# Kernel optimization log

Hardware: AMD Instinct MI355X
Metric: run time of the kernel (lower is better)

Reference implementation:

```python
import jax, jax.numpy as jnp
import numpy as np

NUM_ITER = 2
NUM_SLOTS = 3
D = 64          # slot_dim
MLP_H = 64
C_IN = 512
N = 262144      # number of input features (pixels)
EPS = 1e-8
LN_EPS = 1e-3   # keras LayerNormalization default


def _ln(x, g, b):
    m = jnp.mean(x, axis=-1, keepdims=True)
    v = jnp.var(x, axis=-1, keepdims=True)
    return (x - m) * jax.lax.rsqrt(v + LN_EPS) * g + b


def _gru(x, h, k, rk, bias):
    # keras GRUCell, reset_after=True; bias: [2, 3D] (input bias, recurrent bias)
    xm = x @ k + bias[0]
    hm = h @ rk + bias[1]
    xz, xr, xh = jnp.split(xm, 3, axis=-1)
    hz, hr, hh = jnp.split(hm, 3, axis=-1)
    z = jax.nn.sigmoid(xz + hz)
    r = jax.nn.sigmoid(xr + hr)
    cand = jnp.tanh(xh + r * hh)
    return z * h + (1.0 - z) * cand


def _mlp(s, g, b, W1, b1, W2, b2):
    h = _ln(s, g, b)
    return jax.nn.relu(h @ W1 + b1) @ W2 + b2


def _glorot(key, shape):
    fan_in, fan_out = shape[0], shape[-1]
    lim = np.sqrt(6.0 / (fan_in + fan_out))
    return jax.random.uniform(key, shape, jnp.float32, -lim, lim)


def setup_inputs() -> dict:
    key = jax.random.key(0)
    ks = jax.random.split(key, 24)
    inp = {
        'x': jax.random.normal(ks[0], (N, C_IN), jnp.float32),
        'noise_fg': jax.random.normal(ks[1], (NUM_SLOTS - 1, D), jnp.float32),
        'noise_bg': jax.random.normal(ks[2], (1, D), jnp.float32),
        'ln_g': jnp.ones((C_IN,), jnp.float32),
        'ln_b': jnp.zeros((C_IN,), jnp.float32),
        'mu_fg': _glorot(ks[3], (1, D)),
        'ls_fg': _glorot(ks[4], (1, D)),
        'mu_bg': _glorot(ks[5], (1, D)),
        'ls_bg': _glorot(ks[6], (1, D)),
        'Wk': _glorot(ks[7], (C_IN, D)),
        'Wv': _glorot(ks[8], (C_IN, D)),
        'qfg_g': jnp.ones((D,), jnp.float32), 'qfg_b': jnp.zeros((D,), jnp.float32),
        'qfg_W': _glorot(ks[9], (D, D)),
        'qbg_g': jnp.ones((D,), jnp.float32), 'qbg_b': jnp.zeros((D,), jnp.float32),
        'qbg_W': _glorot(ks[10], (D, D)),
        'grufg_k': _glorot(ks[11], (D, 3 * D)),
        'grufg_rk': _glorot(ks[12], (D, 3 * D)),
        'grufg_bias': jnp.zeros((2, 3 * D), jnp.float32),
        'grubg_k': _glorot(ks[13], (D, 3 * D)),
        'grubg_rk': _glorot(ks[14], (D, 3 * D)),
        'grubg_bias': jnp.zeros((2, 3 * D), jnp.float32),
        'mlpfg_g': jnp.ones((D,), jnp.float32), 'mlpfg_b': jnp.zeros((D,), jnp.float32),
        'mlpfg_W1': _glorot(ks[15], (D, MLP_H)), 'mlpfg_b1': jnp.zeros((MLP_H,), jnp.float32),
        'mlpfg_W2': _glorot(ks[16], (MLP_H, D)), 'mlpfg_b2': jnp.zeros((D,), jnp.float32),
        'mlpbg_g': jnp.ones((D,), jnp.float32), 'mlpbg_b': jnp.zeros((D,), jnp.float32),
        'mlpbg_W1': _glorot(ks[17], (D, MLP_H)), 'mlpbg_b1': jnp.zeros((MLP_H,), jnp.float32),
        'mlpbg_W2': _glorot(ks[18], (MLP_H, D)), 'mlpbg_b2': jnp.zeros((D,), jnp.float32),
    }
    return inp


def reference(x, noise_fg, noise_bg, ln_g, ln_b, mu_fg, ls_fg, mu_bg, ls_bg,
              Wk, Wv, qfg_g, qfg_b, qfg_W, qbg_g, qbg_b, qbg_W,
              grufg_k, grufg_rk, grufg_bias, grubg_k, grubg_rk, grubg_bias,
              mlpfg_g, mlpfg_b, mlpfg_W1, mlpfg_b1, mlpfg_W2, mlpfg_b2,
              mlpbg_g, mlpbg_b, mlpbg_W1, mlpbg_b1, mlpbg_W2, mlpbg_b2):
    x = _ln(x, ln_g, ln_b)
    slots_fg = mu_fg + jnp.exp(ls_fg) * noise_fg      # [K-1, D]
    slots_bg = mu_bg + jnp.exp(ls_bg) * noise_bg      # [1, D]
    k = x @ Wk                                        # [N, D]
    v = x @ Wv                                        # [N, D]
    scale = D ** (-0.5)
    attn = None
    for _ in range(NUM_ITER):
        q_fg = _ln(slots_fg, qfg_g, qfg_b) @ qfg_W * scale
        q_bg = _ln(slots_bg, qbg_g, qbg_b) @ qbg_W * scale
        logits = jnp.concatenate([k @ q_bg.T, k @ q_fg.T], axis=-1)  # [N, K]
        attn = jax.nn.softmax(logits, axis=-1)
        attn_bg, attn_fg = attn[:, 0:1], attn[:, 1:]
        w_bg = attn_bg + EPS
        w_bg = w_bg / jnp.sum(w_bg, axis=-2, keepdims=True)
        upd_bg = w_bg.T @ v                                          # [1, D]
        w_fg = attn_fg + EPS
        w_fg = w_fg / jnp.sum(w_fg, axis=-2, keepdims=True)
        upd_fg = w_fg.T @ v                                          # [K-1, D]
        slots_bg = _gru(upd_bg, slots_bg, grubg_k, grubg_rk, grubg_bias)
        slots_fg = _gru(upd_fg, slots_fg, grufg_k, grufg_rk, grufg_bias)
        slots_bg = slots_bg + _mlp(slots_bg, mlpbg_g, mlpbg_b, mlpbg_W1, mlpbg_b1, mlpbg_W2, mlpbg_b2)
        slots_fg = slots_fg + _mlp(slots_fg, mlpfg_g, mlpfg_b, mlpfg_W1, mlpfg_b1, mlpfg_W2, mlpfg_b2)
    slots = jnp.concatenate([slots_bg, slots_fg], axis=0)            # [K, D]
    return slots, attn.T                                             # [K,D], [K,N]
```

## Files before the change

kernel.cpp:

```cpp
#include <hip/hip_runtime.h>
#include <hip/hip_bf16.h>


#define N_TOK 262144
#define CIN 512
#define TILE_M 64
#define NBLK_A 512
#define NBLK_I2 1024
#define PSTRIDE 1024

typedef __attribute__((ext_vector_type(8))) short short8;
typedef __attribute__((ext_vector_type(4))) float f32x4;

__device__ __forceinline__ unsigned short f2bf(float f) {
    union { float f; unsigned u; } v; v.f = f;
    unsigned r = v.u + 0x7FFFu + ((v.u >> 16) & 1u);
    return (unsigned short)(r >> 16);
}
__device__ __forceinline__ unsigned pkbf(float a, float b) {
    return (unsigned)f2bf(a) | ((unsigned)f2bf(b) << 16);
}
__device__ __forceinline__ float bf2f(unsigned short u) {
    union { unsigned u; float f; } v; v.u = ((unsigned)u) << 16;
    return v.f;
}
__device__ __forceinline__ float sigmoidf_(float x) { return 1.f / (1.f + expf(-x)); }

__device__ __forceinline__ float q_from_slot(float v, const float* __restrict__ g,
                                             const float* __restrict__ b,
                                             const float* __restrict__ W, int lane) {
    float s = v, s2 = v * v;
#pragma unroll
    for (int d = 1; d < 64; d <<= 1) { s += __shfl_xor(s, d); s2 += __shfl_xor(s2, d); }
    float mean = s * (1.f / 64.f);
    float var = s2 * (1.f / 64.f) - mean * mean;
    float rstd = rsqrtf(var + 1e-3f);
    float hl = (v - mean) * rstd * g[lane] + b[lane];
    float acc = 0.f;
    for (int i = 0; i < 64; ++i) acc += __shfl(hl, i) * W[i * 64 + lane];
    return acc * 0.125f;
}

__global__ __launch_bounds__(256) void wt_init_kernel(
    const float* __restrict__ Wk, const float* __restrict__ Wv,
    const float* __restrict__ ln_g, const float* __restrict__ ln_b,
    unsigned short* __restrict__ Wt, float* __restrict__ c12,
    const float* __restrict__ noise_fg, const float* __restrict__ noise_bg,
    const float* __restrict__ mu_fg, const float* __restrict__ ls_fg,
    const float* __restrict__ mu_bg, const float* __restrict__ ls_bg,
    const float* __restrict__ qbg_g, const float* __restrict__ qbg_b, const float* __restrict__ qbg_W,
    const float* __restrict__ qfg_g, const float* __restrict__ qfg_b, const float* __restrict__ qfg_W,
    float* __restrict__ slots_ws, float* __restrict__ q_ws) {
    int t = threadIdx.x;
    if (blockIdx.x < 128) {
        int j = blockIdx.x;
        const float* W = (j < 64) ? Wk : Wv;
        int jc = j & 63;
        float c1 = 0.f, c2 = 0.f;
        for (int i = t; i < 512; i += 256) {
            float wv = W[i * 64 + jc];
            float g = ln_g[i], b = ln_b[i];
            c1 += g * wv; c2 += b * wv;
            Wt[(size_t)j * 512 + i] = f2bf(g * wv);
        }
        __shared__ float s1[4], s2[4];
#pragma unroll
        for (int d = 1; d < 64; d <<= 1) { c1 += __shfl_xor(c1, d); c2 += __shfl_xor(c2, d); }
        if ((t & 63) == 0) { s1[t >> 6] = c1; s2[t >> 6] = c2; }
        __syncthreads();
        if (t == 0) {
            c12[j] = (s1[0] + s1[1]) + (s1[2] + s1[3]);
            c12[128 + j] = (s2[0] + s2[1]) + (s2[2] + s2[3]);
        }
    } else {
        if (t < 192) {
            int s = t >> 6, c = t & 63;
            float v = (s == 0) ? (mu_bg[c] + expf(ls_bg[c]) * noise_bg[c])
                               : (mu_fg[c] + expf(ls_fg[c]) * noise_fg[(s - 1) * 64 + c]);
            slots_ws[t] = v;
            const float* g = s ? qfg_g : qbg_g;
            const float* b = s ? qfg_b : qbg_b;
            const float* W = s ? qfg_W : qbg_W;
            q_ws[t] = q_from_slot(v, g, b, W, c);
        }
    }
}

__global__ __launch_bounds__(256, 2) void phaseA_kernel(
    const float* __restrict__ x, const unsigned short* __restrict__ Wt,
    const float* __restrict__ c12, const float* __restrict__ qv,
    unsigned short* __restrict__ kb, unsigned short* __restrict__ vb,
    float* __restrict__ partials) {
    __shared__ unsigned short SA[TILE_M * CIN];
    __shared__ float q_s[192];
    __shared__ float w_s[64 * 4];
    __shared__ float2 rowstat[64];
    float* kvf = (float*)SA;

    const int t = threadIdx.x;
    const int lane = t & 63;
    const int w = t >> 6;

    if (t < 192) q_s[t] = qv[t];

    short8 bfrag[16][2];
    float c1r[2], c2r[2];
#pragma unroll
    for (int nt = 0; nt < 2; ++nt) {
        int col = w * 32 + nt * 16 + (lane & 15);
        c1r[nt] = c12[col];
        c2r[nt] = c12[128 + col];
#pragma unroll
        for (int kk = 0; kk < 16; ++kk) {
            int off = kk * 32 + ((lane >> 4) << 3);
            bfrag[kk][nt] = *(const short8*)(Wt + (size_t)col * 512 + off);
        }
    }

    float upd_acc = 0.f;
    float sw_acc = 0.f;

    for (int tile = blockIdx.x; tile < N_TOK / TILE_M; tile += NBLK_A) {
        const size_t row0 = (size_t)tile * TILE_M;
        __syncthreads();

#pragma unroll
        for (int p = 0; p < 2; ++p) {
            int r = w * 16 + p * 8 + (lane >> 3);
            int c8 = lane & 7;
            const float4* xr = (const float4*)(x + (row0 + r) * CIN) + c8 * 16;
            char* rowbase = (char*)SA + r * 1024;
            int bb = c8 * 128;
            int sw = (r & 7) << 4;
            float s = 0.f, s2 = 0.f;
#pragma unroll
            for (int i = 0; i < 8; ++i) {
                float4 a = xr[2 * i];
                float4 b = xr[2 * i + 1];
                s += (a.x + a.y) + (a.z + a.w) + (b.x + b.y) + (b.z + b.w);
                s2 = fmaf(a.x, a.x, s2); s2 = fmaf(a.y, a.y, s2);
                s2 = fmaf(a.z, a.z, s2); s2 = fmaf(a.w, a.w, s2);
                s2 = fmaf(b.x, b.x, s2); s2 = fmaf(b.y, b.y, s2);
                s2 = fmaf(b.z, b.z, s2); s2 = fmaf(b.w, b.w, s2);
                uint4 o;
                o.x = pkbf(a.x, a.y); o.y = pkbf(a.z, a.w);
                o.z = pkbf(b.x, b.y); o.w = pkbf(b.z, b.w);
                *(uint4*)(rowbase + ((bb + i * 16) ^ sw)) = o;
            }
#pragma unroll
            for (int d = 1; d < 8; d <<= 1) { s += __shfl_xor(s, d); s2 += __shfl_xor(s2, d); }
            if (c8 == 0) {
                float mean = s * (1.f / 512.f);
                float var = s2 * (1.f / 512.f) - mean * mean;
                float rstd = rsqrtf(var + 1e-3f);
                rowstat[r] = make_float2(rstd, mean * rstd);
            }
        }
        __syncthreads();

        f32x4 acc[4][2];
#pragma unroll
        for (int m = 0; m < 4; ++m) {
            acc[m][0] = (f32x4){0.f, 0.f, 0.f, 0.f};
            acc[m][1] = (f32x4){0.f, 0.f, 0.f, 0.f};
        }
#pragma unroll
        for (int kk = 0; kk < 16; ++kk) {
#pragma unroll
            for (int m = 0; m < 4; ++m) {
                int row = m * 16 + (lane & 15);
                int boff = (kk * 64 + ((lane >> 4) << 4)) ^ ((row & 7) << 4);
                short8 af = *(const short8*)((const char*)SA + row * 1024 + boff);
                acc[m][0] = __builtin_amdgcn_mfma_f32_16x16x32_bf16(af, bfrag[kk][0], acc[m][0], 0, 0, 0);
                acc[m][1] = __builtin_amdgcn_mfma_f32_16x16x32_bf16(af, bfrag[kk][1], acc[m][1], 0, 0, 0);
            }
        }
        __syncthreads();

        float2 rs[16];
#pragma unroll
        for (int m = 0; m < 4; ++m)
#pragma unroll
            for (int j = 0; j < 4; ++j)
                rs[m * 4 + j] = rowstat[m * 16 + ((lane >> 4) << 2) + j];
#pragma unroll
        for (int m = 0; m < 4; ++m)
#pragma unroll
            for (int n = 0; n < 2; ++n)
#pragma unroll
                for (int j = 0; j < 4; ++j) {
                    int row = m * 16 + ((lane >> 4) << 2) + j;
                    int col = w * 32 + n * 16 + (lane & 15);
                    float val = fmaf(rs[m * 4 + j].x, acc[m][n][j],
                                     fmaf(-rs[m * 4 + j].y, c1r[n], c2r[n]));
                    kvf[row * 130 + col] = val;
                }
        __syncthreads();

        {
            int r = t >> 2, q4 = t & 3;
            unsigned short* dst = ((q4 < 2) ? kb : vb) + (row0 + r) * 64 + (q4 & 1) * 32;
            const float* src = &kvf[r * 130 + q4 * 32];
#pragma unroll
            for (int j = 0; j < 32; j += 8) {
                float2 p0 = *(const float2*)(src + j);
                float2 p1 = *(const float2*)(src + j + 2);
                float2 p2 = *(const float2*)(src + j + 4);
                float2 p3 = *(const float2*)(src + j + 6);
                uint4 o;
                o.x = pkbf(p0.x, p0.y);
                o.y = pkbf(p1.x, p1.y);
                o.z = pkbf(p2.x, p2.y);
                o.w = pkbf(p3.x, p3.y);
                *(uint4*)(dst + j) = o;
            }
        }
        if (t < 64) {
            int r = t;
            float l0 = 0.f, l1 = 0.f, l2 = 0.f;
#pragma unroll 8
            for (int c = 0; c < 64; c += 2) {
                float2 kv2 = *(const float2*)&kvf[r * 130 + c];
                l0 += kv2.x * q_s[c] + kv2.y * q_s[c + 1];
                l1 += kv2.x * q_s[64 + c] + kv2.y * q_s[64 + c + 1];
                l2 += kv2.x * q_s[128 + c] + kv2.y * q_s[128 + c + 1];
            }
            float mx = fmaxf(l0, fmaxf(l1, l2));
            float e0 = expf(l0 - mx), e1 = expf(l1 - mx), e2 = expf(l2 - mx);
            float inv = 1.f / (e0 + e1 + e2);
            w_s[r * 4 + 0] = e0 * inv + 1e-8f;
            w_s[r * 4 + 1] = e1 * inv + 1e-8f;
            w_s[r * 4 + 2] = e2 * inv + 1e-8f;
        }
        __syncthreads();

        if (t < 192) {
            int s = t >> 6, c = t & 63;
            float a = 0.f;
            for (int r = 0; r < 64; ++r) a += w_s[r * 4 + s] * kvf[r * 130 + 64 + c];
            upd_acc += a;
        } else if (t < 195) {
            int s = t - 192;
            float a = 0.f;
            for (int r = 0; r < 64; ++r) a += w_s[r * 4 + s];
            sw_acc += a;
        }
    }
    if (t < 192) partials[(size_t)t * PSTRIDE + blockIdx.x] = upd_acc;
    else if (t < 195) partials[(size_t)t * PSTRIDE + blockIdx.x] = sw_acc;
}

__global__ __launch_bounds__(256) void iter2_kernel(
    const unsigned short* __restrict__ kb, const unsigned short* __restrict__ vb,
    const float* __restrict__ qv, float* __restrict__ attn_out, float* __restrict__ partials) {
    __shared__ float q_s[192];
    __shared__ float w_s[256 * 4];
    __shared__ unsigned short v_lds[256 * 64];
    int t = threadIdx.x;
    if (t < 192) q_s[t] = qv[t];
    __syncthreads();
    size_t r = (size_t)blockIdx.x * 256 + t;
    const unsigned short* krow = kb + r * 64;
    float l0 = 0.f, l1 = 0.f, l2 = 0.f;
#pragma unroll
    for (int i = 0; i < 8; ++i) {
        uint4 u = *(const uint4*)(krow + i * 8);
        unsigned uu[4] = {u.x, u.y, u.z, u.w};
#pragma unroll
        for (int p = 0; p < 4; ++p) {
            float fa = bf2f((unsigned short)(uu[p] & 0xffffu));
            float fb = bf2f((unsigned short)(uu[p] >> 16));
            int c = i * 8 + p * 2;
            l0 += fa * q_s[c] + fb * q_s[c + 1];
            l1 += fa * q_s[64 + c] + fb * q_s[64 + c + 1];
            l2 += fa * q_s[128 + c] + fb * q_s[128 + c + 1];
        }
    }
    float mx = fmaxf(l0, fmaxf(l1, l2));
    float e0 = expf(l0 - mx), e1 = expf(l1 - mx), e2 = expf(l2 - mx);
    float inv = 1.f / (e0 + e1 + e2);
    float a0 = e0 * inv, a1 = e1 * inv, a2 = e2 * inv;
    attn_out[r] = a0;
    attn_out[(size_t)N_TOK + r] = a1;
    attn_out[2 * (size_t)N_TOK + r] = a2;
    w_s[t * 4 + 0] = a0 + 1e-8f;
    w_s[t * 4 + 1] = a1 + 1e-8f;
    w_s[t * 4 + 2] = a2 + 1e-8f;
    {
        const uint4* vr = (const uint4*)(vb + r * 64);
        uint4* vl = (uint4*)(v_lds + t * 64);
#pragma unroll
        for (int i = 0; i < 8; ++i) vl[i] = vr[i];
    }
    __syncthreads();
    if (t < 192) {
        int s = t >> 6, c = t & 63;
        float part = 0.f;
        for (int r2 = 0; r2 < 256; ++r2) part += w_s[r2 * 4 + s] * bf2f(v_lds[r2 * 64 + c]);
        partials[(size_t)t * PSTRIDE + blockIdx.x] = part;
    } else if (t < 195) {
        int s = t - 192;
        float part = 0.f;
        for (int r2 = 0; r2 < 256; ++r2) part += w_s[r2 * 4 + s];
        partials[(size_t)t * PSTRIDE + blockIdx.x] = part;
    }
}

__global__ __launch_bounds__(256) void reduce_kernel(const float* __restrict__ partials,
                                                     int nblk, float* __restrict__ reduced) {
    int col = blockIdx.x, t = threadIdx.x;
    float a = 0.f;
    for (int b = t; b < nblk; b += 256) a += partials[(size_t)col * PSTRIDE + b];
#pragma unroll
    for (int d = 1; d < 64; d <<= 1) a += __shfl_xor(a, d);
    __shared__ float ws_[4];
    if ((t & 63) == 0) ws_[t >> 6] = a;
    __syncthreads();
    if (t == 0) reduced[col] = (ws_[0] + ws_[1]) + (ws_[2] + ws_[3]);
}

__global__ __launch_bounds__(256) void update_kernel(
    const float* __restrict__ reduced,
    float* __restrict__ slots_ws, float* __restrict__ q_ws,
    const float* __restrict__ gbg_k, const float* __restrict__ gbg_rk, const float* __restrict__ gbg_bias,
    const float* __restrict__ gfg_k, const float* __restrict__ gfg_rk, const float* __restrict__ gfg_bias,
    const float* __restrict__ mbg_g, const float* __restrict__ mbg_b, const float* __restrict__ mbg_W1,
    const float* __restrict__ mbg_b1, const float* __restrict__ mbg_W2, const float* __restrict__ mbg_b2,
    const float* __restrict__ mfg_g, const float* __restrict__ mfg_b, const float* __restrict__ mfg_W1,
    const float* __restrict__ mfg_b1, const float* __restrict__ mfg_W2, const float* __restrict__ mfg_b2,
    const float* __restrict__ qbg_g, const float* __restrict__ qbg_b, const float* __restrict__ qbg_W,
    const float* __restrict__ qfg_g, const float* __restrict__ qfg_b, const float* __restrict__ qfg_W,
    int compute_q, float* __restrict__ out_slots) {
    __shared__ float upd[192], hslots[192], swv[3];
    __shared__ float xm[192], hm[192], gout[64], lnv[64], hid[64];
    int t = threadIdx.x;
    if (t < 192) { hslots[t] = slots_ws[t]; upd[t] = reduced[t]; }
    else if (t < 195) swv[t - 192] = reduced[t];
    __syncthreads();
    if (t < 192) upd[t] = upd[t] / swv[t >> 6];
    __syncthreads();

    for (int s = 0; s < 3; ++s) {
        const float* K = s ? gfg_k : gbg_k;
        const float* RK = s ? gfg_rk : gbg_rk;
        const float* BS = s ? gfg_bias : gbg_bias;
        if (t < 192) {
            float ax = BS[t], ah = BS[192 + t];
            const float* us = upd + s * 64;
            const float* hs = hslots + s * 64;
            for (int i = 0; i < 64; ++i) {
                ax += us[i] * K[i * 192 + t];
                ah += hs[i] * RK[i * 192 + t];
            }
            xm[t] = ax; hm[t] = ah;
        }
        __syncthreads();
        if (t < 64) {
            float z = sigmoidf_(xm[t] + hm[t]);
            float rg = sigmoidf_(xm[64 + t] + hm[64 + t]);
            float cand = tanhf(xm[128 + t] + rg * hm[128 + t]);
            gout[t] = z * hslots[s * 64 + t] + (1.f - z) * cand;
        }
        __syncthreads();
        const float* MG = s ? mfg_g : mbg_g;
        const float* MB = s ? mfg_b : mbg_b;
        const float* MW1 = s ? mfg_W1 : mbg_W1;
        const float* MB1 = s ? mfg_b1 : mbg_b1;
        const float* MW2 = s ? mfg_W2 : mbg_W2;
        const float* MB2 = s ? mfg_b2 : mbg_b2;
        if (t < 64) {
            float v = gout[t];
            float su = v, sq = v * v;
#pragma unroll
            for (int d = 1; d < 64; d <<= 1) { su += __shfl_xor(su, d); sq += __shfl_xor(sq, d); }
            float mean = su * (1.f / 64.f), var = sq * (1.f / 64.f) - mean * mean;
            float rstd = rsqrtf(var + 1e-3f);
            lnv[t] = (v - mean) * rstd * MG[t] + MB[t];
        }
        __syncthreads();
        if (t < 64) {
            float a = MB1[t];
            for (int i = 0; i < 64; ++i) a += lnv[i] * MW1[i * 64 + t];
            hid[t] = fmaxf(a, 0.f);
        }
        __syncthreads();
        if (t < 64) {
            float a = MB2[t];
            for (int i = 0; i < 64; ++i) a += hid[i] * MW2[i * 64 + t];
            hslots[s * 64 + t] = gout[t] + a;
        }
        __syncthreads();
    }
    if (t < 192) {
        slots_ws[t] = hslots[t];
        if (out_slots) out_slots[t] = hslots[t];
        if (compute_q) {
            int s = t >> 6, lane = t & 63;
            const float* g = s ? qfg_g : qbg_g;
            const float* b = s ? qfg_b : qbg_b;
            const float* W = s ? qfg_W : qbg_W;
            q_ws[t] = q_from_slot(hslots[t], g, b, W, lane);
        }
    }
}

extern "C" void kernel_launch(void* const* d_in, const int* in_sizes, int n_in,
                              void* d_out, int out_size, void* d_ws, size_t ws_size,
                              hipStream_t stream) {
    const float* x        = (const float*)d_in[0];
    const float* noise_fg = (const float*)d_in[1];
    const float* noise_bg = (const float*)d_in[2];
    const float* ln_g     = (const float*)d_in[3];
    const float* ln_b     = (const float*)d_in[4];
    const float* mu_fg    = (const float*)d_in[5];
    const float* ls_fg    = (const float*)d_in[6];
    const float* mu_bg    = (const float*)d_in[7];
    const float* ls_bg    = (const float*)d_in[8];
    const float* Wk       = (const float*)d_in[9];
    const float* Wv       = (const float*)d_in[10];
    const float* qfg_g    = (const float*)d_in[11];
    const float* qfg_b    = (const float*)d_in[12];
    const float* qfg_W    = (const float*)d_in[13];
    const float* qbg_g    = (const float*)d_in[14];
    const float* qbg_b    = (const float*)d_in[15];
    const float* qbg_W    = (const float*)d_in[16];
    const float* gfg_k    = (const float*)d_in[17];
    const float* gfg_rk   = (const float*)d_in[18];
    const float* gfg_bias = (const float*)d_in[19];
    const float* gbg_k    = (const float*)d_in[20];
    const float* gbg_rk   = (const float*)d_in[21];
    const float* gbg_bias = (const float*)d_in[22];
    const float* mfg_g    = (const float*)d_in[23];
    const float* mfg_b    = (const float*)d_in[24];
    const float* mfg_W1   = (const float*)d_in[25];
    const float* mfg_b1   = (const float*)d_in[26];
    const float* mfg_W2   = (const float*)d_in[27];
    const float* mfg_b2   = (const float*)d_in[28];
    const float* mbg_g    = (const float*)d_in[29];
    const float* mbg_b    = (const float*)d_in[30];
    const float* mbg_W1   = (const float*)d_in[31];
    const float* mbg_b1   = (const float*)d_in[32];
    const float* mbg_W2   = (const float*)d_in[33];
    const float* mbg_b2   = (const float*)d_in[34];

    char* ws = (char*)d_ws;
    unsigned short* Wt = (unsigned short*)ws;
    float* c12 = (float*)(ws + 131072);
    unsigned short* kb = (unsigned short*)(ws + 132096);
    unsigned short* vb = kb + (size_t)N_TOK * 64;
    char* ws2 = ws + 132096 + (size_t)2 * N_TOK * 64 * 2;
    float* slots_ws = (float*)ws2;
    float* q_ws = slots_ws + 192;
    float* reduced = q_ws + 192;
    float* partials = reduced + 256;

    float* out = (float*)d_out;

    wt_init_kernel<<<dim3(129), dim3(256), 0, stream>>>(
        Wk, Wv, ln_g, ln_b, Wt, c12,
        noise_fg, noise_bg, mu_fg, ls_fg, mu_bg, ls_bg,
        qbg_g, qbg_b, qbg_W, qfg_g, qfg_b, qfg_W, slots_ws, q_ws);
    phaseA_kernel<<<dim3(NBLK_A), dim3(256), 0, stream>>>(x, Wt, c12, q_ws, kb, vb, partials);
    reduce_kernel<<<dim3(195), dim3(256), 0, stream>>>(partials, NBLK_A, reduced);
    update_kernel<<<dim3(1), dim3(256), 0, stream>>>(reduced, slots_ws, q_ws,
        gbg_k, gbg_rk, gbg_bias, gfg_k, gfg_rk, gfg_bias,
        mbg_g, mbg_b, mbg_W1, mbg_b1, mbg_W2, mbg_b2,
        mfg_g, mfg_b, mfg_W1, mfg_b1, mfg_W2, mfg_b2,
        qbg_g, qbg_b, qbg_W, qfg_g, qfg_b, qfg_W, 1, (float*)nullptr);
    iter2_kernel<<<dim3(NBLK_I2), dim3(256), 0, stream>>>(kb, vb, q_ws, out + 192, partials);
    reduce_kernel<<<dim3(195), dim3(256), 0, stream>>>(partials, NBLK_I2, reduced);
    update_kernel<<<dim3(1), dim3(256), 0, stream>>>(reduced, slots_ws, q_ws,
        gbg_k, gbg_rk, gbg_bias, gfg_k, gfg_rk, gfg_bias,
        mbg_g, mbg_b, mbg_W1, mbg_b1, mbg_W2, mbg_b2,
        mfg_g, mfg_b, mfg_W1, mfg_b1, mfg_W2, mfg_b2,
        qbg_g, qbg_b, qbg_W, qfg_g, qfg_b, qfg_W, 0, out);
}
```

Baseline: 240.4 us.

## Double phaseA block to 512 threads with each wave owning 16 output columns

```diff
diff --git a/kernel.cpp b/kernel.cpp
--- a/kernel.cpp
+++ b/kernel.cpp
@@ -86,7 +86,7 @@
     }
 }
 
-__global__ __launch_bounds__(256, 2) void phaseA_kernel(
+__global__ __launch_bounds__(512, 4) void phaseA_kernel(
     const float* __restrict__ x, const unsigned short* __restrict__ Wt,
     const float* __restrict__ c12, const float* __restrict__ qv,
     unsigned short* __restrict__ kb, unsigned short* __restrict__ vb,
@@ -103,18 +103,14 @@
 
     if (t < 192) q_s[t] = qv[t];
 
-    short8 bfrag[16][2];
-    float c1r[2], c2r[2];
-#pragma unroll
-    for (int nt = 0; nt < 2; ++nt) {
-        int col = w * 32 + nt * 16 + (lane & 15);
-        c1r[nt] = c12[col];
-        c2r[nt] = c12[128 + col];
-#pragma unroll
-        for (int kk = 0; kk < 16; ++kk) {
-            int off = kk * 32 + ((lane >> 4) << 3);
-            bfrag[kk][nt] = *(const short8*)(Wt + (size_t)col * 512 + off);
-        }
+    const int col = w * 16 + (lane & 15);
+    const float c1r = c12[col];
+    const float c2r = c12[128 + col];
+    short8 bfrag[16];
+#pragma unroll
+    for (int kk = 0; kk < 16; ++kk) {
+        int off = kk * 32 + ((lane >> 4) << 3);
+        bfrag[kk] = *(const short8*)(Wt + (size_t)col * 512 + off);
     }
 
     float upd_acc = 0.f;
@@ -124,10 +120,9 @@
         const size_t row0 = (size_t)tile * TILE_M;
         __syncthreads();
 
-#pragma unroll
-        for (int p = 0; p < 2; ++p) {
-            int r = w * 16 + p * 8 + (lane >> 3);
-            int c8 = lane & 7;
+        {
+            int r = t >> 3;
+            int c8 = t & 7;
             const float4* xr = (const float4*)(x + (row0 + r) * CIN) + c8 * 16;
             char* rowbase = (char*)SA + r * 1024;
             int bb = c8 * 128;
@@ -158,12 +153,9 @@
         }
         __syncthreads();
 
-        f32x4 acc[4][2];
-#pragma unroll
-        for (int m = 0; m < 4; ++m) {
-            acc[m][0] = (f32x4){0.f, 0.f, 0.f, 0.f};
-            acc[m][1] = (f32x4){0.f, 0.f, 0.f, 0.f};
-        }
+        f32x4 acc[4];
+#pragma unroll
+        for (int m = 0; m < 4; ++m) acc[m] = (f32x4){0.f, 0.f, 0.f, 0.f};
 #pragma unroll
         for (int kk = 0; kk < 16; ++kk) {
 #pragma unroll
@@ -171,49 +163,40 @@
                 int row = m * 16 + (lane & 15);
                 int boff = (kk * 64 + ((lane >> 4) << 4)) ^ ((row & 7) << 4);
                 short8 af = *(const short8*)((const char*)SA + row * 1024 + boff);
-                acc[m][0] = __builtin_amdgcn_mfma_f32_16x16x32_bf16(af, bfrag[kk][0], acc[m][0], 0, 0, 0);
-                acc[m][1] = __builtin_amdgcn_mfma_f32_16x16x32_bf16(af, bfrag[kk][1], acc[m][1], 0, 0, 0);
-            }
-        }
-        __syncthreads();
-
-        float2 rs[16];
-#pragma unroll
-        for (int m = 0; m < 4; ++m)
-#pragma unroll
-            for (int j = 0; j < 4; ++j)
-                rs[m * 4 + j] = rowstat[m * 16 + ((lane >> 4) << 2) + j];
-#pragma unroll
-        for (int m = 0; m < 4; ++m)
-#pragma unroll
-            for (int n = 0; n < 2; ++n)
-#pragma unroll
-                for (int j = 0; j < 4; ++j) {
-                    int row = m * 16 + ((lane >> 4) << 2) + j;
-                    int col = w * 32 + n * 16 + (lane & 15);
-                    float val = fmaf(rs[m * 4 + j].x, acc[m][n][j],
-                                     fmaf(-rs[m * 4 + j].y, c1r[n], c2r[n]));
-                    kvf[row * 130 + col] = val;
-                }
+                acc[m] = __builtin_amdgcn_mfma_f32_16x16x32_bf16(af, bfrag[kk], acc[m], 0, 0, 0);
+            }
+        }
+        __syncthreads();
+
+#pragma unroll
+        for (int m = 0; m < 4; ++m) {
+#pragma unroll
+            for (int j = 0; j < 4; ++j) {
+                int row = m * 16 + ((lane >> 4) << 2) + j;
+                float2 rs = rowstat[row];
+                float val = fmaf(rs.x, acc[m][j], fmaf(-rs.y, c1r, c2r));
+                kvf[row * 130 + col] = val;
+            }
+        }
         __syncthreads();
 
         {
-            int r = t >> 2, q4 = t & 3;
-            unsigned short* dst = ((q4 < 2) ? kb : vb) + (row0 + r) * 64 + (q4 & 1) * 32;
-            const float* src = &kvf[r * 130 + q4 * 32];
-#pragma unroll
-            for (int j = 0; j < 32; j += 8) {
-                float2 p0 = *(const float2*)(src + j);
-                float2 p1 = *(const float2*)(src + j + 2);
-                float2 p2 = *(const float2*)(src + j + 4);
-                float2 p3 = *(const float2*)(src + j + 6);
-                uint4 o;
-                o.x = pkbf(p0.x, p0.y);
-                o.y = pkbf(p1.x, p1.y);
-                o.z = pkbf(p2.x, p2.y);
-                o.w = pkbf(p3.x, p3.y);
-                *(uint4*)(dst + j) = o;
-            }
+            int r = t >> 3, h = t & 7;
+            const float* src = &kvf[r * 130 + h * 16];
+            unsigned short* dst = (h < 4) ? (kb + (row0 + r) * 64 + h * 16)
+                                          : (vb + (row0 + r) * 64 + (h - 4) * 16);
+            uint4 o0, o1;
+            float2 p;
+            p = *(const float2*)(src + 0);  o0.x = pkbf(p.x, p.y);
+            p = *(const float2*)(src + 2);  o0.y = pkbf(p.x, p.y);
+            p = *(const float2*)(src + 4);  o0.z = pkbf(p.x, p.y);
+            p = *(const float2*)(src + 6);  o0.w = pkbf(p.x, p.y);
+            p = *(const float2*)(src + 8);  o1.x = pkbf(p.x, p.y);
+            p = *(const float2*)(src + 10); o1.y = pkbf(p.x, p.y);
+            p = *(const float2*)(src + 12); o1.z = pkbf(p.x, p.y);
+            p = *(const float2*)(src + 14); o1.w = pkbf(p.x, p.y);
+            *(uint4*)dst = o0;
+            *(uint4*)(dst + 8) = o1;
         }
         if (t < 64) {
             int r = t;
@@ -460,7 +443,7 @@
         Wk, Wv, ln_g, ln_b, Wt, c12,
         noise_fg, noise_bg, mu_fg, ls_fg, mu_bg, ls_bg,
         qbg_g, qbg_b, qbg_W, qfg_g, qfg_b, qfg_W, slots_ws, q_ws);
-    phaseA_kernel<<<dim3(NBLK_A), dim3(256), 0, stream>>>(x, Wt, c12, q_ws, kb, vb, partials);
+    phaseA_kernel<<<dim3(NBLK_A), dim3(512), 0, stream>>>(x, Wt, c12, q_ws, kb, vb, partials);
     reduce_kernel<<<dim3(195), dim3(256), 0, stream>>>(partials, NBLK_A, reduced);
     update_kernel<<<dim3(1), dim3(256), 0, stream>>>(reduced, slots_ws, q_ws,
         gbg_k, gbg_rk, gbg_bias, gfg_k, gfg_rk, gfg_bias,
```

After: 300.9 us. 1.25x slower.

## Prefetch next tile's input rows into registers and reload weight fragments per k-step

Applied to the files above, without the earlier changes.

```diff
diff --git a/kernel.cpp b/kernel.cpp
--- a/kernel.cpp
+++ b/kernel.cpp
@@ -5,6 +5,7 @@
 #define N_TOK 262144
 #define CIN 512
 #define TILE_M 64
+#define NT (N_TOK / TILE_M)
 #define NBLK_A 512
 #define NBLK_I2 1024
 #define PSTRIDE 1024
@@ -103,60 +104,78 @@
 
     if (t < 192) q_s[t] = qv[t];
 
-    short8 bfrag[16][2];
-    float c1r[2], c2r[2];
-#pragma unroll
-    for (int nt = 0; nt < 2; ++nt) {
-        int col = w * 32 + nt * 16 + (lane & 15);
-        c1r[nt] = c12[col];
-        c2r[nt] = c12[128 + col];
-#pragma unroll
-        for (int kk = 0; kk < 16; ++kk) {
-            int off = kk * 32 + ((lane >> 4) << 3);
-            bfrag[kk][nt] = *(const short8*)(Wt + (size_t)col * 512 + off);
-        }
-    }
+    const int col0 = w * 32 + (lane & 15);
+    const float c1r[2] = { c12[col0], c12[col0 + 16] };
+    const float c2r[2] = { c12[128 + col0], c12[128 + col0 + 16] };
+
+    const int rA = w * 16 + (lane >> 3);
+    const int c8 = lane & 7;
+
+    const unsigned short* wb0 = Wt + (size_t)col0 * 512;
+    const unsigned short* wb1 = wb0 + 16 * 512;
+    const int woff = (lane >> 4) << 3;
 
     float upd_acc = 0.f;
     float sw_acc = 0.f;
 
-    for (int tile = blockIdx.x; tile < N_TOK / TILE_M; tile += NBLK_A) {
+    __syncthreads();
+
+    auto do_pass = [&](const float4* buf, int r) {
+        char* rowbase = (char*)SA + r * 1024;
+        const int bb = c8 * 128;
+        const int sw = (r & 7) << 4;
+        float s = 0.f, s2 = 0.f;
+#pragma unroll
+        for (int i = 0; i < 8; ++i) {
+            float4 a = buf[2 * i];
+            float4 b = buf[2 * i + 1];
+            s += (a.x + a.y) + (a.z + a.w) + (b.x + b.y) + (b.z + b.w);
+            s2 = fmaf(a.x, a.x, s2); s2 = fmaf(a.y, a.y, s2);
+            s2 = fmaf(a.z, a.z, s2); s2 = fmaf(a.w, a.w, s2);
+            s2 = fmaf(b.x, b.x, s2); s2 = fmaf(b.y, b.y, s2);
+            s2 = fmaf(b.z, b.z, s2); s2 = fmaf(b.w, b.w, s2);
+            uint4 o;
+            o.x = pkbf(a.x, a.y); o.y = pkbf(a.z, a.w);
+            o.z = pkbf(b.x, b.y); o.w = pkbf(b.z, b.w);
+            *(uint4*)(rowbase + ((bb + i * 16) ^ sw)) = o;
+        }
+#pragma unroll
+        for (int d = 1; d < 8; d <<= 1) { s += __shfl_xor(s, d); s2 += __shfl_xor(s2, d); }
+        if (c8 == 0) {
+            float mean = s * (1.f / 512.f);
+            float var = s2 * (1.f / 512.f) - mean * mean;
+            float rstd = rsqrtf(var + 1e-3f);
+            rowstat[r] = make_float2(rstd, mean * rstd);
+        }
+    };
+
+    float4 xa[16], xb[16];
+    {
+        const float4* xr = (const float4*)(x + ((size_t)blockIdx.x * TILE_M + rA) * CIN) + c8 * 16;
+#pragma unroll
+        for (int i = 0; i < 16; ++i) xa[i] = xr[i];
+    }
+
+    for (int tile = blockIdx.x; tile < NT; tile += NBLK_A) {
         const size_t row0 = (size_t)tile * TILE_M;
-        __syncthreads();
-
-#pragma unroll
-        for (int p = 0; p < 2; ++p) {
-            int r = w * 16 + p * 8 + (lane >> 3);
-            int c8 = lane & 7;
-            const float4* xr = (const float4*)(x + (row0 + r) * CIN) + c8 * 16;
-            char* rowbase = (char*)SA + r * 1024;
-            int bb = c8 * 128;
-            int sw = (r & 7) << 4;
-            float s = 0.f, s2 = 0.f;
-#pragma unroll
-            for (int i = 0; i < 8; ++i) {
-                float4 a = xr[2 * i];
-                float4 b = xr[2 * i + 1];
-                s += (a.x + a.y) + (a.z + a.w) + (b.x + b.y) + (b.z + b.w);
-                s2 = fmaf(a.x, a.x, s2); s2 = fmaf(a.y, a.y, s2);
-                s2 = fmaf(a.z, a.z, s2); s2 = fmaf(a.w, a.w, s2);
-                s2 = fmaf(b.x, b.x, s2); s2 = fmaf(b.y, b.y, s2);
-                s2 = fmaf(b.z, b.z, s2); s2 = fmaf(b.w, b.w, s2);
-                uint4 o;
-                o.x = pkbf(a.x, a.y); o.y = pkbf(a.z, a.w);
-                o.z = pkbf(b.x, b.y); o.w = pkbf(b.z, b.w);
-                *(uint4*)(rowbase + ((bb + i * 16) ^ sw)) = o;
-            }
-#pragma unroll
-            for (int d = 1; d < 8; d <<= 1) { s += __shfl_xor(s, d); s2 += __shfl_xor(s2, d); }
-            if (c8 == 0) {
-                float mean = s * (1.f / 512.f);
-                float var = s2 * (1.f / 512.f) - mean * mean;
-                float rstd = rsqrtf(var + 1e-3f);
-                rowstat[r] = make_float2(rstd, mean * rstd);
-            }
-        }
-        __syncthreads();
+        const int nxt = tile + NBLK_A;
+
+        __builtin_amdgcn_s_barrier();
+
+        {
+            const float4* xr = (const float4*)(x + (row0 + rA + 8) * CIN) + c8 * 16;
+#pragma unroll
+            for (int i = 0; i < 16; ++i) xb[i] = xr[i];
+        }
+        do_pass(xa, rA);
+        do_pass(xb, rA + 8);
+        if (nxt < NT) {
+            const float4* xr = (const float4*)(x + ((size_t)nxt * TILE_M + rA) * CIN) + c8 * 16;
+#pragma unroll
+            for (int i = 0; i < 16; ++i) xa[i] = xr[i];
+        }
+        asm volatile("s_waitcnt lgkmcnt(0)" ::: "memory");
+        __builtin_amdgcn_s_barrier();
 
         f32x4 acc[4][2];
 #pragma unroll
@@ -166,16 +185,18 @@
         }
 #pragma unroll
         for (int kk = 0; kk < 16; ++kk) {
+            short8 bf0 = *(const short8*)(wb0 + kk * 32 + woff);
+            short8 bf1 = *(const short8*)(wb1 + kk * 32 + woff);
 #pragma unroll
             for (int m = 0; m < 4; ++m) {
                 int row = m * 16 + (lane & 15);
                 int boff = (kk * 64 + ((lane >> 4) << 4)) ^ ((row & 7) << 4);
                 short8 af = *(const short8*)((const char*)SA + row * 1024 + boff);
-                acc[m][0] = __builtin_amdgcn_mfma_f32_16x16x32_bf16(af, bfrag[kk][0], acc[m][0], 0, 0, 0);
-                acc[m][1] = __builtin_amdgcn_mfma_f32_16x16x32_bf16(af, bfrag[kk][1], acc[m][1], 0, 0, 0);
+                acc[m][0] = __builtin_amdgcn_mfma_f32_16x16x32_bf16(af, bf0, acc[m][0], 0, 0, 0);
+                acc[m][1] = __builtin_amdgcn_mfma_f32_16x16x32_bf16(af, bf1, acc[m][1], 0, 0, 0);
             }
         }
-        __syncthreads();
+        __builtin_amdgcn_s_barrier();
 
         float2 rs[16];
 #pragma unroll
@@ -190,12 +211,13 @@
 #pragma unroll
                 for (int j = 0; j < 4; ++j) {
                     int row = m * 16 + ((lane >> 4) << 2) + j;
-                    int col = w * 32 + n * 16 + (lane & 15);
+                    int col = col0 + n * 16;
                     float val = fmaf(rs[m * 4 + j].x, acc[m][n][j],
                                      fmaf(-rs[m * 4 + j].y, c1r[n], c2r[n]));
                     kvf[row * 130 + col] = val;
                 }
-        __syncthreads();
+        asm volatile("s_waitcnt lgkmcnt(0)" ::: "memory");
+        __builtin_amdgcn_s_barrier();
 
         {
             int r = t >> 2, q4 = t & 3;
@@ -232,7 +254,8 @@
             w_s[r * 4 + 1] = e1 * inv + 1e-8f;
             w_s[r * 4 + 2] = e2 * inv + 1e-8f;
         }
-        __syncthreads();
+        asm volatile("s_waitcnt lgkmcnt(0)" ::: "memory");
+        __builtin_amdgcn_s_barrier();
 
         if (t < 192) {
             int s = t >> 6, c = t & 63;
```

New measurement: 267.9 us. 11.4% more time.

## Stage GRU/MLP weights into LDS and prewarm them in L2 during reduce

Applied to the files above, without the earlier changes.

```diff
diff --git a/kernel.cpp b/kernel.cpp
--- a/kernel.cpp
+++ b/kernel.cpp
@@ -11,6 +11,8 @@
 
 typedef __attribute__((ext_vector_type(8))) short short8;
 typedef __attribute__((ext_vector_type(4))) float f32x4;
+typedef __attribute__((address_space(3))) void lds_t;
+typedef const __attribute__((address_space(1))) void gbl_t;
 
 __device__ __forceinline__ unsigned short f2bf(float f) {
     union { float f; unsigned u; } v; v.f = f;
@@ -306,8 +308,14 @@
     }
 }
 
-__global__ __launch_bounds__(256) void reduce_kernel(const float* __restrict__ partials,
-                                                     int nblk, float* __restrict__ reduced) {
+__global__ __launch_bounds__(256) void reduce_kernel(
+    const float* __restrict__ partials, int nblk, float* __restrict__ reduced,
+    const float* __restrict__ w0, const float* __restrict__ w1,
+    const float* __restrict__ w2, const float* __restrict__ w3,
+    const float* __restrict__ w4, const float* __restrict__ w5,
+    const float* __restrict__ w6, const float* __restrict__ w7,
+    const float* __restrict__ w8, const float* __restrict__ w9,
+    float* __restrict__ warmsink) {
     int col = blockIdx.x, t = threadIdx.x;
     float a = 0.f;
     for (int b = t; b < nblk; b += 256) a += partials[(size_t)col * PSTRIDE + b];
@@ -317,9 +325,33 @@
     if ((t & 63) == 0) ws_[t >> 6] = a;
     __syncthreads();
     if (t == 0) reduced[col] = (ws_[0] + ws_[1]) + (ws_[2] + ws_[3]);
-}
-
-__global__ __launch_bounds__(256) void update_kernel(
+
+    if (col < 10) {
+        const float* wp; int wn;
+        switch (col) {
+            case 0: wp = w0; wn = 12288; break;
+            case 1: wp = w1; wn = 12288; break;
+            case 2: wp = w2; wn = 12288; break;
+            case 3: wp = w3; wn = 12288; break;
+            case 4: wp = w4; wn = 4096; break;
+            case 5: wp = w5; wn = 4096; break;
+            case 6: wp = w6; wn = 4096; break;
+            case 7: wp = w7; wn = 4096; break;
+            case 8: wp = w8; wn = 4096; break;
+            default: wp = w9; wn = 4096; break;
+        }
+        float acc = 0.f;
+        for (int i = 4 * t; i < wn; i += 1024) {
+            float4 v = *(const float4*)(wp + i);
+            acc += (v.x + v.y) + (v.z + v.w);
+        }
+#pragma unroll
+        for (int d = 1; d < 64; d <<= 1) acc += __shfl_xor(acc, d);
+        if ((t & 63) == 0) warmsink[col * 4 + (t >> 6)] = acc;
+    }
+}
+
+__global__ __launch_bounds__(512, 1) void update_kernel(
     const float* __restrict__ reduced,
     float* __restrict__ slots_ws, float* __restrict__ q_ws,
     const float* __restrict__ gbg_k, const float* __restrict__ gbg_rk, const float* __restrict__ gbg_bias,
@@ -331,9 +363,28 @@
     const float* __restrict__ qbg_g, const float* __restrict__ qbg_b, const float* __restrict__ qbg_W,
     const float* __restrict__ qfg_g, const float* __restrict__ qfg_b, const float* __restrict__ qfg_W,
     int compute_q, float* __restrict__ out_slots) {
-    __shared__ float upd[192], hslots[192], swv[3];
+    __shared__ __align__(16) float Kl[64 * 192];
+    __shared__ __align__(16) float RKl[64 * 192];
+    __shared__ __align__(16) float W1l[64 * 64];
+    __shared__ __align__(16) float W2l[64 * 64];
+    __shared__ float upd[192], hslots[192], swv[4];
     __shared__ float xm[192], hm[192], gout[64], lnv[64], hid[64];
-    int t = threadIdx.x;
+    const int t = threadIdx.x;
+
+#define STAGE(src_, dst_, nfloat_)                                                      \
+    {                                                                                   \
+        _Pragma("unroll")                                                               \
+        for (int i_ = 0; i_ < (nfloat_) / 2048; ++i_)                                   \
+            __builtin_amdgcn_global_load_lds((gbl_t*)((src_) + 4 * (i_ * 512 + t)),     \
+                                             (lds_t*)((dst_) + 4 * (i_ * 512 + t)),     \
+                                             16, 0, 0);                                 \
+    }
+
+    STAGE(gbg_k, Kl, 12288);
+    STAGE(gbg_rk, RKl, 12288);
+    STAGE(mbg_W1, W1l, 4096);
+    STAGE(mbg_W2, W2l, 4096);
+
     if (t < 192) { hslots[t] = slots_ws[t]; upd[t] = reduced[t]; }
     else if (t < 195) swv[t - 192] = reduced[t];
     __syncthreads();
@@ -341,20 +392,26 @@
     __syncthreads();
 
     for (int s = 0; s < 3; ++s) {
-        const float* K = s ? gfg_k : gbg_k;
-        const float* RK = s ? gfg_rk : gbg_rk;
         const float* BS = s ? gfg_bias : gbg_bias;
         if (t < 192) {
-            float ax = BS[t], ah = BS[192 + t];
+            float a = BS[t];
             const float* us = upd + s * 64;
+#pragma unroll 8
+            for (int i = 0; i < 64; ++i) a = fmaf(us[i], Kl[i * 192 + t], a);
+            xm[t] = a;
+        } else if (t < 384) {
+            int c = t - 192;
+            float a = BS[192 + c];
             const float* hs = hslots + s * 64;
-            for (int i = 0; i < 64; ++i) {
-                ax += us[i] * K[i * 192 + t];
-                ah += hs[i] * RK[i * 192 + t];
-            }
-            xm[t] = ax; hm[t] = ah;
-        }
-        __syncthreads();
+#pragma unroll 8
+            for (int i = 0; i < 64; ++i) a = fmaf(hs[i], RKl[i * 192 + c], a);
+            hm[c] = a;
+        }
+        __syncthreads();
+        if (s == 0) {
+            STAGE(gfg_k, Kl, 12288);
+            STAGE(gfg_rk, RKl, 12288);
+        }
         if (t < 64) {
             float z = sigmoidf_(xm[t] + hm[t]);
             float rg = sigmoidf_(xm[64 + t] + hm[64 + t]);
@@ -364,9 +421,7 @@
         __syncthreads();
         const float* MG = s ? mfg_g : mbg_g;
         const float* MB = s ? mfg_b : mbg_b;
-        const float* MW1 = s ? mfg_W1 : mbg_W1;
         const float* MB1 = s ? mfg_b1 : mbg_b1;
-        const float* MW2 = s ? mfg_W2 : mbg_W2;
         const float* MB2 = s ? mfg_b2 : mbg_b2;
         if (t < 64) {
             float v = gout[t];
@@ -380,16 +435,23 @@
         __syncthreads();
         if (t < 64) {
             float a = MB1[t];
-            for (int i = 0; i < 64; ++i) a += lnv[i] * MW1[i * 64 + t];
+#pragma unroll 8
+            for (int i = 0; i < 64; ++i) a = fmaf(lnv[i], W1l[i * 64 + t], a);
             hid[t] = fmaxf(a, 0.f);
         }
         __syncthreads();
         if (t < 64) {
             float a = MB2[t];
-            for (int i = 0; i < 64; ++i) a += hid[i] * MW2[i * 64 + t];
+#pragma unroll 8
+            for (int i = 0; i < 64; ++i) a = fmaf(hid[i], W2l[i * 64 + t], a);
             hslots[s * 64 + t] = gout[t] + a;
         }
         __syncthreads();
+        if (s == 0) {
+            STAGE(mfg_W1, W1l, 4096);
+            STAGE(mfg_W2, W2l, 4096);
+            __syncthreads();
+        }
     }
     if (t < 192) {
         slots_ws[t] = hslots[t];
@@ -402,6 +464,7 @@
             q_ws[t] = q_from_slot(hslots[t], g, b, W, lane);
         }
     }
+#undef STAGE
 }
 
 extern "C" void kernel_launch(void* const* d_in, const int* in_sizes, int n_in,
@@ -453,6 +516,7 @@
     float* q_ws = slots_ws + 192;
     float* reduced = q_ws + 192;
     float* partials = reduced + 256;
+    float* warmsink = partials + (size_t)195 * PSTRIDE;
 
     float* out = (float*)d_out;
 
@@ -461,15 +525,17 @@
         noise_fg, noise_bg, mu_fg, ls_fg, mu_bg, ls_bg,
         qbg_g, qbg_b, qbg_W, qfg_g, qfg_b, qfg_W, slots_ws, q_ws);
     phaseA_kernel<<<dim3(NBLK_A), dim3(256), 0, stream>>>(x, Wt, c12, q_ws, kb, vb, partials);
-    reduce_kernel<<<dim3(195), dim3(256), 0, stream>>>(partials, NBLK_A, reduced);
-    update_kernel<<<dim3(1), dim3(256), 0, stream>>>(reduced, slots_ws, q_ws,
+    reduce_kernel<<<dim3(195), dim3(256), 0, stream>>>(partials, NBLK_A, reduced,
+        gbg_k, gbg_rk, gfg_k, gfg_rk, mbg_W1, mbg_W2, mfg_W1, mfg_W2, qbg_W, qfg_W, warmsink);
+    update_kernel<<<dim3(1), dim3(512), 0, stream>>>(reduced, slots_ws, q_ws,
         gbg_k, gbg_rk, gbg_bias, gfg_k, gfg_rk, gfg_bias,
         mbg_g, mbg_b, mbg_W1, mbg_b1, mbg_W2, mbg_b2,
         mfg_g, mfg_b, mfg_W1, mfg_b1, mfg_W2, mfg_b2,
         qbg_g, qbg_b, qbg_W, qfg_g, qfg_b, qfg_W, 1, (float*)nullptr);
     iter2_kernel<<<dim3(NBLK_I2), dim3(256), 0, stream>>>(kb, vb, q_ws, out + 192, partials);
-    reduce_kernel<<<dim3(195), dim3(256), 0, stream>>>(partials, NBLK_I2, reduced);
-    update_kernel<<<dim3(1), dim3(256), 0, stream>>>(reduced, slots_ws, q_ws,
+    reduce_kernel<<<dim3(195), dim3(256), 0, stream>>>(partials, NBLK_I2, reduced,
+        gbg_k, gbg_rk, gfg_k, gfg_rk, mbg_W1, mbg_W2, mfg_W1, mfg_W2, qbg_W, qfg_W, warmsink);
+    update_kernel<<<dim3(1), dim3(512), 0, stream>>>(reduced, slots_ws, q_ws,
         gbg_k, gbg_rk, gbg_bias, gfg_k, gfg_rk, gfg_bias,
         mbg_g, mbg_b, mbg_W1, mbg_b1, mbg_W2, mbg_b2,
         mfg_g, mfg_b, mfg_W1, mfg_b1, mfg_W2, mfg_b2,
```

New measurement: 247.2 us. 1.03x slower.
